# Performance work log

Hardware: AMD Instinct MI355X
Metric: run time of the kernel (lower is better)

The kernel has to match this reference:

```python
import jax, jax.numpy as jnp
import numpy as np

VOCAB, D, BLOCK = 32000, 1024, 2048
B, S = 4, 2048

def setup_inputs() -> dict:
    key = jax.random.key(0)
    ks = jax.random.split(key, 12)
    s = 0.02
    return {
        "x": jax.random.randint(ks[0], (B, S), 0, VOCAB),
        "tok_emb": jax.random.normal(ks[1], (VOCAB, D), jnp.float32) * s,
        "pos_emb": jax.random.normal(ks[2], (BLOCK, D), jnp.float32) * s,
        "Wq": jax.random.normal(ks[3], (D, D), jnp.float32) * s,
        "bq": jnp.zeros((D,), jnp.float32),
        "Wk": jax.random.normal(ks[4], (D, D), jnp.float32) * s,
        "bk": jnp.zeros((D,), jnp.float32),
        "Wv": jax.random.normal(ks[5], (D, D), jnp.float32) * s,
        "bv": jnp.zeros((D,), jnp.float32),
        "Wfc": jax.random.normal(ks[6], (VOCAB, D), jnp.float32) * s,
        "bfc": jnp.zeros((VOCAB,), jnp.float32),
    }

def reference(x, tok_emb, pos_emb, Wq, bq, Wk, bk, Wv, bv, Wfc, bfc):
    # embeddings: token lookup + learned positional
    h = tok_emb[x] + pos_emb[jnp.arange(x.shape[1])][None, :, :]  # [B,S,D]
    Q = h @ Wq.T + bq
    K = h @ Wk.T + bk
    V = h @ Wv.T + bv
    scale = 1.0 / jnp.sqrt(jnp.float32(Q.shape[-1]))
    scores = jnp.einsum('bqd,bkd->bqk', Q, K) * scale  # [B,S,S]
    attn = jax.nn.softmax(scores, axis=-1)
    out = jnp.einsum('bqk,bkd->bqd', attn, V)
    return out @ Wfc.T + bfc  # [B,S,VOCAB]
```

## Files before the change

kernel.cpp:

```cpp
#include <hip/hip_runtime.h>
#include <hip/hip_bf16.h>
#include <stdint.h>

typedef __bf16 bf16x8 __attribute__((ext_vector_type(8)));
typedef float f32x4 __attribute__((ext_vector_type(4)));
typedef unsigned short u16x8 __attribute__((ext_vector_type(8)));

#define DEVINL static __device__ __forceinline__

DEVINL unsigned short f2bf(float f) {
  unsigned u = __builtin_bit_cast(unsigned, f);
  unsigned r = (u + 0x7FFFu + ((u >> 16) & 1u)) >> 16;
  return (unsigned short)r;
}
DEVINL float bf2f(unsigned short u) {
  return __builtin_bit_cast(float, ((unsigned)u) << 16);
}

DEVINL void gload_lds16(const unsigned short* g, unsigned short* l) {
  __builtin_amdgcn_global_load_lds(
      (const __attribute__((address_space(1))) void*)g,
      (__attribute__((address_space(3))) void*)l, 16, 0, 0);
}

__global__ __launch_bounds__(256) void embed_kernel(
    const int* __restrict__ x, const float* __restrict__ tok,
    const float* __restrict__ pos, unsigned short* __restrict__ hb)
{
  const int bs = blockIdx.x;
  const int s  = bs & 2047;
  const long trow = (long)x[bs] * 1024;
  const int d = threadIdx.x * 4;
  const float4 t = *(const float4*)(tok + trow + d);
  const float4 p = *(const float4*)(pos + (long)s * 1024 + d);
  ushort4 o;
  o.x = f2bf(t.x + p.x);
  o.y = f2bf(t.y + p.y);
  o.z = f2bf(t.z + p.z);
  o.w = f2bf(t.w + p.w);
  *(ushort4*)(hb + (long)bs * 1024 + d) = o;
}

__global__ __launch_bounds__(256) void cvt4_kernel(
    const float* __restrict__ wq, const float* __restrict__ wk,
    const float* __restrict__ wv, const float* __restrict__ wfc,
    unsigned short* __restrict__ out)
{
  for (long i = blockIdx.x * blockDim.x + threadIdx.x; i < 8978432;
       i += (long)gridDim.x * blockDim.x) {
    const float* src;
    long off;
    if (i < 262144)       { src = wq;  off = i; }
    else if (i < 524288)  { src = wk;  off = i - 262144; }
    else if (i < 786432)  { src = wv;  off = i - 524288; }
    else                  { src = wfc; off = i - 786432; }
    float4 v = ((const float4*)src)[off];
    ushort4 o;
    o.x = f2bf(v.x); o.y = f2bf(v.y); o.z = f2bf(v.z); o.w = f2bf(v.w);
    ((ushort4*)out)[i] = o;
  }
}

template<int OUTMODE>
__global__ __launch_bounds__(256) void gemm_bt(
    const unsigned short* __restrict__ A, const unsigned short* __restrict__ B,
    void* __restrict__ Cout, const float* __restrict__ bias,
    float scale, int M, int N, int K,
    long sA, long sB, long sC, int Mb, long tStride, int mapMode)
{
  __shared__ __align__(16) unsigned short lA[128 * 32];
  __shared__ __align__(16) unsigned short lB[128 * 32];
  const int tid = threadIdx.x, wid = tid >> 6, lane = tid & 63;
  int bx, by, bz;
  if (mapMode == 0) {
    bx = blockIdx.x; by = blockIdx.y; bz = blockIdx.z;
  } else {
    const int bid = blockIdx.x;
    const int g = bid & 7, jj = bid >> 3;
    bz = g >> 1;
    by = (g & 1) * 8 + (jj & 7);
    bx = jj >> 3;
  }
  A += (long)bz * sA;
  B += (long)bz * sB;
  const int bm = by * 128, bn = bx * 128;

  const int c0 = wid * 64 + lane, c1 = c0 + 256;
  const unsigned short* gA0 = A + (long)(bm + (c0 >> 2)) * K + (c0 & 3) * 8;
  const unsigned short* gA1 = A + (long)(bm + (c1 >> 2)) * K + (c1 & 3) * 8;
  const unsigned short* gB0 = B + (long)(bn + (c0 >> 2)) * K + (c0 & 3) * 8;
  const unsigned short* gB1 = B + (long)(bn + (c1 >> 2)) * K + (c1 & 3) * 8;
  unsigned short* lA0 = lA + wid * 512;
  unsigned short* lA1 = lA + 2048 + wid * 512;
  unsigned short* lB0 = lB + wid * 512;
  unsigned short* lB1 = lB + 2048 + wid * 512;

  const int wr = (wid >> 1) * 64, wc = (wid & 1) * 64;
  const int lr = lane & 15, lk = (lane >> 4) * 8;

  f32x4 acc[4][4] = {};
  const int nk = K >> 5;
  for (int kt = 0; kt < nk; ++kt) {
    const int ko = kt << 5;
    gload_lds16(gA0 + ko, lA0);
    gload_lds16(gA1 + ko, lA1);
    gload_lds16(gB0 + ko, lB0);
    gload_lds16(gB1 + ko, lB1);
    __syncthreads();
    bf16x8 af[4], bg[4];
#pragma unroll
    for (int m = 0; m < 4; ++m)
      af[m] = *(const bf16x8*)(const void*)(lA + (wr + m * 16 + lr) * 32 + lk);
#pragma unroll
    for (int n = 0; n < 4; ++n)
      bg[n] = *(const bf16x8*)(const void*)(lB + (wc + n * 16 + lr) * 32 + lk);
#pragma unroll
    for (int m = 0; m < 4; ++m)
#pragma unroll
      for (int n = 0; n < 4; ++n)
        acc[m][n] = __builtin_amdgcn_mfma_f32_16x16x32_bf16(af[m], bg[n],
                                                            acc[m][n], 0, 0, 0);
    __syncthreads();
  }

  const int r0 = bm + wr + ((lane >> 4) << 2);
  const int cbase = bn + wc + lr;
#pragma unroll
  for (int n = 0; n < 4; ++n) {
    const int col = cbase + n * 16;
    const float bv = bias ? bias[col] : 0.f;
#pragma unroll
    for (int m = 0; m < 4; ++m) {
      const int row0 = r0 + m * 16;
      if (OUTMODE == 2) {
        float* C = (float*)Cout + (long)bz * sC;
#pragma unroll
        for (int i = 0; i < 4; ++i)
          C[(long)(row0 + i) * N + col] = acc[m][n][i] * scale + bv;
      } else if (OUTMODE == 0) {
        unsigned short* C = (unsigned short*)Cout + (long)bz * sC;
#pragma unroll
        for (int i = 0; i < 4; ++i)
          C[(long)(row0 + i) * N + col] = f2bf(acc[m][n][i] * scale + bv);
      } else {
        unsigned short* C = (unsigned short*)Cout;
        const int b = row0 / Mb;
        const int srow = row0 - b * Mb;
        ushort4 o;
        o.x = f2bf(acc[m][n][0] * scale + bv);
        o.y = f2bf(acc[m][n][1] * scale + bv);
        o.z = f2bf(acc[m][n][2] * scale + bv);
        o.w = f2bf(acc[m][n][3] * scale + bv);
        *(ushort4*)(C + (long)b * tStride + (long)col * Mb + srow) = o;
      }
    }
  }
}

__global__ __launch_bounds__(256) void qkv_bt(
    const unsigned short* __restrict__ A, const unsigned short* __restrict__ B,
    unsigned short* __restrict__ Qb, unsigned short* __restrict__ Kb,
    unsigned short* __restrict__ Vt,
    const float* __restrict__ bq, const float* __restrict__ bk,
    const float* __restrict__ bv)
{
  constexpr int K = 1024;
  __shared__ __align__(16) unsigned short lA[128 * 32];
  __shared__ __align__(16) unsigned short lB[128 * 32];
  const int tid = threadIdx.x, wid = tid >> 6, lane = tid & 63;
  const int bid = blockIdx.x;
  const int g = bid & 7, j = bid >> 3;
  const int bm = (g * 8 + (j & 7)) * 128;
  const int bn = (j >> 3) * 128;
  const int sector = bn >> 10;
  const int bnl = bn & 1023;

  const int c0 = wid * 64 + lane, c1 = c0 + 256;
  const unsigned short* gA0 = A + (long)(bm + (c0 >> 2)) * K + (c0 & 3) * 8;
  const unsigned short* gA1 = A + (long)(bm + (c1 >> 2)) * K + (c1 & 3) * 8;
  const unsigned short* gB0 = B + (long)(bn + (c0 >> 2)) * K + (c0 & 3) * 8;
  const unsigned short* gB1 = B + (long)(bn + (c1 >> 2)) * K + (c1 & 3) * 8;
  unsigned short* lA0 = lA + wid * 512;
  unsigned short* lA1 = lA + 2048 + wid * 512;
  unsigned short* lB0 = lB + wid * 512;
  unsigned short* lB1 = lB + 2048 + wid * 512;

  const int wr = (wid >> 1) * 64, wc = (wid & 1) * 64;
  const int lr = lane & 15, lk = (lane >> 4) * 8;

  f32x4 acc[4][4] = {};
  for (int kt = 0; kt < 32; ++kt) {
    const int ko = kt << 5;
    gload_lds16(gA0 + ko, lA0);
    gload_lds16(gA1 + ko, lA1);
    gload_lds16(gB0 + ko, lB0);
    gload_lds16(gB1 + ko, lB1);
    __syncthreads();
    bf16x8 af[4], bg[4];
#pragma unroll
    for (int m = 0; m < 4; ++m)
      af[m] = *(const bf16x8*)(const void*)(lA + (wr + m * 16 + lr) * 32 + lk);
#pragma unroll
    for (int n = 0; n < 4; ++n)
      bg[n] = *(const bf16x8*)(const void*)(lB + (wc + n * 16 + lr) * 32 + lk);
#pragma unroll
    for (int m = 0; m < 4; ++m)
#pragma unroll
      for (int n = 0; n < 4; ++n)
        acc[m][n] = __builtin_amdgcn_mfma_f32_16x16x32_bf16(af[m], bg[n],
                                                            acc[m][n], 0, 0, 0);
    __syncthreads();
  }

  const float* bias = (sector == 0) ? bq : (sector == 1) ? bk : bv;
  const int r0 = bm + wr + ((lane >> 4) << 2);
  const int cbase = bnl + wc + lr;
#pragma unroll
  for (int n = 0; n < 4; ++n) {
    const int col = cbase + n * 16;
    const float bb = bias[col];
#pragma unroll
    for (int m = 0; m < 4; ++m) {
      const int row0 = r0 + m * 16;
      if (sector == 2) {
        const int b = row0 >> 11;
        const int srow = row0 & 2047;
        ushort4 o;
        o.x = f2bf(acc[m][n][0] + bb);
        o.y = f2bf(acc[m][n][1] + bb);
        o.z = f2bf(acc[m][n][2] + bb);
        o.w = f2bf(acc[m][n][3] + bb);
        *(ushort4*)(Vt + (long)b * (1024L * 2048) + (long)col * 2048 + srow) = o;
      } else {
        unsigned short* C = (sector == 0) ? Qb : Kb;
#pragma unroll
        for (int i = 0; i < 4; ++i)
          C[(long)(row0 + i) * 1024 + col] = f2bf(acc[m][n][i] + bb);
      }
    }
  }
}

__global__ __launch_bounds__(256) void softmax_kernel(unsigned short* __restrict__ S)
{
  unsigned short* row = S + (long)blockIdx.x * 2048;
  const int t = threadIdx.x, lane = t & 63, wid = t >> 6;
  __shared__ float redm[4], reds[4];
  u16x8 raw = ((const u16x8*)row)[t];
  float v[8];
#pragma unroll
  for (int j = 0; j < 8; ++j) v[j] = bf2f(raw[j]);
  float mx = v[0];
#pragma unroll
  for (int j = 1; j < 8; ++j) mx = fmaxf(mx, v[j]);
#pragma unroll
  for (int off = 32; off; off >>= 1) mx = fmaxf(mx, __shfl_xor(mx, off, 64));
  if (lane == 0) redm[wid] = mx;
  __syncthreads();
  mx = fmaxf(fmaxf(redm[0], redm[1]), fmaxf(redm[2], redm[3]));
  float s = 0.f;
#pragma unroll
  for (int j = 0; j < 8; ++j) { v[j] = __expf(v[j] - mx); s += v[j]; }
#pragma unroll
  for (int off = 32; off; off >>= 1) s += __shfl_xor(s, off, 64);
  if (lane == 0) reds[wid] = s;
  __syncthreads();
  s = reds[0] + reds[1] + reds[2] + reds[3];
  const float inv = 1.f / s;
  u16x8 o;
#pragma unroll
  for (int j = 0; j < 8; ++j) o[j] = f2bf(v[j] * inv);
  ((u16x8*)row)[t] = o;
}

DEVINL bf16x8 ldfrag(const unsigned short* p, int row, int kx) {
  return *(const bf16x8*)((const char*)p + row * 128 + kx);
}

#define BARSB() do { __builtin_amdgcn_s_barrier(); \
                     __builtin_amdgcn_sched_barrier(0); } while (0)
#define LGK0() asm volatile("s_waitcnt lgkmcnt(0)")
#define VM6()  asm volatile("s_waitcnt vmcnt(6)")

#define MF16(rb, aArr, bArr) do { \
  _Pragma("unroll") for (int m_ = 0; m_ < 4; ++m_) \
  _Pragma("unroll") for (int n_ = 0; n_ < 4; ++n_) \
    acc[(rb) + m_][n_] = __builtin_amdgcn_mfma_f32_16x16x32_bf16( \
        aArr[m_], bArr[n_], acc[(rb) + m_][n_], 0, 0, 0); \
} while (0)

#define STG_A(b, h, gk) do { \
  const char* s_ = srcA + (h) * 262144 + (long)(((gk) & 15)) * 128; \
  gload_lds16((const unsigned short*)(s_ + la0), \
              dA + (b) * 16384 + (h) * 8192 + dO0); \
  gload_lds16((const unsigned short*)(s_ + la1), \
              dA + (b) * 16384 + (h) * 8192 + dO1); } while (0)
#define STG_B(b, h, gk) do { \
  int t_ = (gk) >> 4; if (t_ >= len) t_ = len - 1; \
  const char* s_ = Bbase + ((long)(bnStart + t_) << 19) + \
                   (h) * 262144 + (long)(((gk) & 15)) * 128; \
  gload_lds16((const unsigned short*)(s_ + la0), \
              dB + (b) * 16384 + (h) * 8192 + dO0); \
  gload_lds16((const unsigned short*)(s_ + la1), \
              dB + (b) * 16384 + (h) * 8192 + dO1); } while (0)

#define KTILE(BUF, S1, S2, S3, S4) do { \
  bf16x8 b0_[4], b1_[4], aA_[4], aB_[4], aC_[4], aD_[4]; \
  _Pragma("unroll") for (int n = 0; n < 4; ++n) { \
    b0_[n] = ldfrag(dB + (BUF) * 16384, wn * 64 + n * 16 + lr, kx0); \
    b1_[n] = ldfrag(dB + (BUF) * 16384, wn * 64 + n * 16 + lr, kx1); } \
  _Pragma("unroll") for (int m = 0; m < 4; ++m) \
    aA_[m] = ldfrag(dA + (BUF) * 16384, wm * 128 + m * 16 + lr, kx0); \
  S1; \
  BARSB(); LGK0(); __builtin_amdgcn_s_setprio(1); \
  MF16(0, aA_, b0_); \
  __builtin_amdgcn_s_setprio(0); BARSB(); \
  _Pragma("unroll") for (int m = 0; m < 4; ++m) { \
    aB_[m] = ldfrag(dA + (BUF) * 16384, wm * 128 + (4 + m) * 16 + lr, kx0); \
    aC_[m] = ldfrag(dA + (BUF) * 16384, wm * 128 + (4 + m) * 16 + lr, kx1); } \
  S2; \
  BARSB(); LGK0(); __builtin_amdgcn_s_setprio(1); \
  MF16(4, aB_, b0_); \
  __builtin_amdgcn_s_setprio(0); BARSB(); \
  _Pragma("unroll") for (int m = 0; m < 4; ++m) \
    aD_[m] = ldfrag(dA + (BUF) * 16384, wm * 128 + m * 16 + lr, kx1); \
  S3; \
  BARSB(); LGK0(); __builtin_amdgcn_s_setprio(1); \
  MF16(4, aC_, b1_); \
  __builtin_amdgcn_s_setprio(0); BARSB(); \
  S4; VM6(); \
  BARSB(); LGK0(); __builtin_amdgcn_s_setprio(1); \
  MF16(0, aD_, b1_); \
  __builtin_amdgcn_s_setprio(0); BARSB(); \
} while (0)

__global__ __launch_bounds__(512, 2) void gemm256_fc(
    const unsigned short* __restrict__ A, const unsigned short* __restrict__ B,
    float* __restrict__ C, const float* __restrict__ bias)
{
  constexpr int N = 32000;
  __shared__ __align__(16) unsigned short lds[65536];
  const int tid = threadIdx.x, wid = tid >> 6, lane = tid & 63;
  const int wm = wid >> 2, wn = wid & 3;
  const int lr = lane & 15;
  const int kq = (lane >> 4) << 4;
  const int xr = (lane & 7) << 4;
  const int kx0 = kq ^ xr;
  const int kx1 = (64 | kq) ^ xr;

  const int bid = blockIdx.x;
  const int g = bid & 7;
  const int j = bid >> 3;
  const int bm = g * 4 + (j & 3);
  const int q = j >> 2;
  const int bnStart = (q < 5) ? 16 * q : 80 + (q - 5) * 15;
  const int len = (q < 5) ? 16 : 15;

  const int loff0 = wid * 1024 + lane * 16;
  const int loff1 = loff0 + 8192;
  const int r0 = loff0 >> 7, r1 = loff1 >> 7;
  const int c0 = (loff0 & 127) ^ ((r0 & 7) << 4);
  const int c1 = (loff1 & 127) ^ ((r1 & 7) << 4);
  const long la0 = (long)r0 * 2048 + c0;
  const long la1 = (long)r1 * 2048 + c1;
  const char* srcA = (const char*)A + ((long)bm << 19);
  const char* Bbase = (const char*)B;
  unsigned short* dA = lds;
  unsigned short* dB = lds + 32768;
  const int dO0 = wid * 512, dO1 = 4096 + wid * 512;

  f32x4 acc[8][4] = {};
  float bv[4];
#pragma unroll
  for (int n = 0; n < 4; ++n)
    bv[n] = bias[(long)bnStart * 256 + wn * 64 + n * 16 + lr];

  STG_B(0, 0, 0); STG_B(0, 1, 0); STG_A(0, 0, 0); STG_A(0, 1, 0);
  STG_B(1, 0, 1); STG_B(1, 1, 1); STG_A(1, 0, 1);
  VM6();
  BARSB();

  for (int t = 0; t < len; ++t) {
#pragma unroll 1
    for (int it = 0; it < 8; ++it) {
      const int gk = t * 16 + 2 * it;
      KTILE(0, STG_A(1, 1, gk + 1), STG_B(0, 0, gk + 2), STG_B(0, 1, gk + 2),
            STG_A(0, 0, gk + 2));
      KTILE(1, STG_A(0, 1, gk + 2), STG_B(1, 0, gk + 3), STG_B(1, 1, gk + 3),
            STG_A(1, 0, gk + 3));
    }
    const long bnRow = ((long)bnStart + t) * 256;
    const int q4 = (lane >> 4) * 4;
#pragma unroll
    for (int m = 0; m < 8; ++m) {
      const long row = (long)bm * 256 + wm * 128 + m * 16 + q4;
#pragma unroll
      for (int i = 0; i < 4; ++i) {
        float* orow = C + (row + i) * (long)N;
#pragma unroll
        for (int n = 0; n < 4; ++n)
          __builtin_nontemporal_store(acc[m][n][i] + bv[n],
                                      &orow[bnRow + wn * 64 + n * 16 + lr]);
      }
    }
    VM6();
    const int tn = (t + 1 < len) ? t + 1 : t;
#pragma unroll
    for (int n = 0; n < 4; ++n)
      bv[n] = bias[((long)bnStart + tn) * 256 + wn * 64 + n * 16 + lr];
#pragma unroll
    for (int m = 0; m < 8; ++m)
#pragma unroll
      for (int n = 0; n < 4; ++n)
        acc[m][n] = f32x4{0.f, 0.f, 0.f, 0.f};
  }
}

extern "C" void kernel_launch(void* const* d_in, const int* in_sizes, int n_in,
                              void* d_out, int out_size, void* d_ws, size_t ws_size,
                              hipStream_t stream)
{
  const int*   x   = (const int*)d_in[0];
  const float* tok = (const float*)d_in[1];
  const float* pos = (const float*)d_in[2];
  const float* Wq  = (const float*)d_in[3];
  const float* bq  = (const float*)d_in[4];
  const float* Wk  = (const float*)d_in[5];
  const float* bk  = (const float*)d_in[6];
  const float* Wv  = (const float*)d_in[7];
  const float* bv  = (const float*)d_in[8];
  const float* Wfc = (const float*)d_in[9];
  const float* bfc = (const float*)d_in[10];
  float* out = (float*)d_out;

  char* ws = (char*)d_ws;
  unsigned short* hb   = (unsigned short*)(ws);
  unsigned short* Wqb  = (unsigned short*)(ws + 16777216);
  unsigned short* Wfcb = (unsigned short*)(ws + 23068672);
  unsigned short* Qb   = (unsigned short*)(ws + 88604672);
  unsigned short* Kb   = (unsigned short*)(ws + 105381888);
  unsigned short* Vt   = (unsigned short*)(ws + 122159104);
  unsigned short* Sc   = (unsigned short*)(ws + 138936320);
  unsigned short* AO   = hb;

  embed_kernel<<<8192, 256, 0, stream>>>(x, tok, pos, hb);
  cvt4_kernel<<<2048, 256, 0, stream>>>(Wq, Wk, Wv, Wfc, Wqb);

  dim3 blk(256);
  qkv_bt<<<dim3(1536), blk, 0, stream>>>(hb, Wqb, Qb, Kb, Vt, bq, bk, bv);
  gemm_bt<0><<<dim3(1024), blk, 0, stream>>>(Qb, Kb, Sc, nullptr, 0.03125f,
      2048, 2048, 1024, 2048L * 1024, 2048L * 1024, 2048L * 2048, 0, 0, 1);
  softmax_kernel<<<8192, 256, 0, stream>>>(Sc);
  gemm_bt<0><<<dim3(512), blk, 0, stream>>>(Sc, Vt, AO, nullptr, 1.f,
      2048, 1024, 2048, 2048L * 2048, 1024L * 2048, 2048L * 1024, 0, 0, 1);
  gemm256_fc<<<dim3(256), dim3(512), 0, stream>>>(AO, Wfcb, out, bfc);
}
```

Baseline: 774.0 us.

## Overlap weight conversion with embedding and score GEMM via fused launches

Splits the fp32-to-bf16 weight conversion so the QKV weights are converted by extra blocks in the embedding kernel, while the large Wfc conversion runs in extra blocks of a new scores GEMM kernel. This hides the memory-bound conversion behind other work and removes one launch. The scores GEMM becomes a specialized copy of the generic gemm_bt with constants baked in. The risk is that conversion blocks compete for bandwidth and compute units with the GEMM, and block scheduling order may serialize them anyway.

```diff
diff --git a/kernel.cpp b/kernel.cpp
--- a/kernel.cpp
+++ b/kernel.cpp
@@ -23,10 +23,27 @@
       (__attribute__((address_space(3))) void*)l, 16, 0, 0);
 }
 
-__global__ __launch_bounds__(256) void embed_kernel(
+__global__ __launch_bounds__(256) void embed_cvtq_kernel(
     const int* __restrict__ x, const float* __restrict__ tok,
-    const float* __restrict__ pos, unsigned short* __restrict__ hb)
-{
+    const float* __restrict__ pos, unsigned short* __restrict__ hb,
+    const float* __restrict__ wq, const float* __restrict__ wk,
+    const float* __restrict__ wv, unsigned short* __restrict__ wqkvb)
+{
+  if (blockIdx.x >= 8192) {
+    const int b = blockIdx.x - 8192;
+    for (long i = (long)b * 256 + threadIdx.x; i < 786432; i += 512 * 256) {
+      const float* src;
+      long off;
+      if (i < 262144)      { src = wq; off = i; }
+      else if (i < 524288) { src = wk; off = i - 262144; }
+      else                 { src = wv; off = i - 524288; }
+      float4 v = ((const float4*)src)[off];
+      ushort4 o;
+      o.x = f2bf(v.x); o.y = f2bf(v.y); o.z = f2bf(v.z); o.w = f2bf(v.w);
+      ((ushort4*)wqkvb)[i] = o;
+    }
+    return;
+  }
   const int bs = blockIdx.x;
   const int s  = bs & 2047;
   const long trow = (long)x[bs] * 1024;
@@ -39,26 +56,6 @@
   o.z = f2bf(t.z + p.z);
   o.w = f2bf(t.w + p.w);
   *(ushort4*)(hb + (long)bs * 1024 + d) = o;
-}
-
-__global__ __launch_bounds__(256) void cvt4_kernel(
-    const float* __restrict__ wq, const float* __restrict__ wk,
-    const float* __restrict__ wv, const float* __restrict__ wfc,
-    unsigned short* __restrict__ out)
-{
-  for (long i = blockIdx.x * blockDim.x + threadIdx.x; i < 8978432;
-       i += (long)gridDim.x * blockDim.x) {
-    const float* src;
-    long off;
-    if (i < 262144)       { src = wq;  off = i; }
-    else if (i < 524288)  { src = wk;  off = i - 262144; }
-    else if (i < 786432)  { src = wv;  off = i - 524288; }
-    else                  { src = wfc; off = i - 786432; }
-    float4 v = ((const float4*)src)[off];
-    ushort4 o;
-    o.x = f2bf(v.x); o.y = f2bf(v.y); o.z = f2bf(v.z); o.w = f2bf(v.w);
-    ((ushort4*)out)[i] = o;
-  }
 }
 
 template<int OUTMODE>
@@ -153,6 +150,87 @@
         o.w = f2bf(acc[m][n][3] * scale + bv);
         *(ushort4*)(C + (long)b * tStride + (long)col * Mb + srow) = o;
       }
+    }
+  }
+}
+
+__global__ __launch_bounds__(256) void scores_cvt_kernel(
+    const unsigned short* __restrict__ Qb, const unsigned short* __restrict__ Kb,
+    unsigned short* __restrict__ Sc,
+    const float* __restrict__ wfc, unsigned short* __restrict__ wfcb)
+{
+  __shared__ __align__(16) unsigned short lA[128 * 32];
+  __shared__ __align__(16) unsigned short lB[128 * 32];
+  if (blockIdx.x < 1024) {
+    for (long i = (long)blockIdx.x * 256 + threadIdx.x; i < 8192000;
+         i += 1024 * 256) {
+      float4 v = ((const float4*)wfc)[i];
+      ushort4 o;
+      o.x = f2bf(v.x); o.y = f2bf(v.y); o.z = f2bf(v.z); o.w = f2bf(v.w);
+      ((ushort4*)wfcb)[i] = o;
+    }
+    return;
+  }
+  constexpr int K = 1024, N = 2048;
+  const int tid = threadIdx.x, wid = tid >> 6, lane = tid & 63;
+  const int bid = blockIdx.x - 1024;
+  const int g = bid & 7, jj = bid >> 3;
+  const int bz = g >> 1;
+  const int by = (g & 1) * 8 + (jj & 7);
+  const int bx = jj >> 3;
+  const unsigned short* A = Qb + (long)bz * (2048L * 1024);
+  const unsigned short* B = Kb + (long)bz * (2048L * 1024);
+  unsigned short* C = Sc + (long)bz * (2048L * 2048);
+  const int bm = by * 128, bn = bx * 128;
+
+  const int c0 = wid * 64 + lane, c1 = c0 + 256;
+  const unsigned short* gA0 = A + (long)(bm + (c0 >> 2)) * K + (c0 & 3) * 8;
+  const unsigned short* gA1 = A + (long)(bm + (c1 >> 2)) * K + (c1 & 3) * 8;
+  const unsigned short* gB0 = B + (long)(bn + (c0 >> 2)) * K + (c0 & 3) * 8;
+  const unsigned short* gB1 = B + (long)(bn + (c1 >> 2)) * K + (c1 & 3) * 8;
+  unsigned short* lA0 = lA + wid * 512;
+  unsigned short* lA1 = lA + 2048 + wid * 512;
+  unsigned short* lB0 = lB + wid * 512;
+  unsigned short* lB1 = lB + 2048 + wid * 512;
+
+  const int wr = (wid >> 1) * 64, wc = (wid & 1) * 64;
+  const int lr = lane & 15, lk = (lane >> 4) * 8;
+
+  f32x4 acc[4][4] = {};
+  for (int kt = 0; kt < 32; ++kt) {
+    const int ko = kt << 5;
+    gload_lds16(gA0 + ko, lA0);
+    gload_lds16(gA1 + ko, lA1);
+    gload_lds16(gB0 + ko, lB0);
+    gload_lds16(gB1 + ko, lB1);
+    __syncthreads();
+    bf16x8 af[4], bg[4];
+#pragma unroll
+    for (int m = 0; m < 4; ++m)
+      af[m] = *(const bf16x8*)(const void*)(lA + (wr + m * 16 + lr) * 32 + lk);
+#pragma unroll
+    for (int n = 0; n < 4; ++n)
+      bg[n] = *(const bf16x8*)(const void*)(lB + (wc + n * 16 + lr) * 32 + lk);
+#pragma unroll
+    for (int m = 0; m < 4; ++m)
+#pragma unroll
+      for (int n = 0; n < 4; ++n)
+        acc[m][n] = __builtin_amdgcn_mfma_f32_16x16x32_bf16(af[m], bg[n],
+                                                            acc[m][n], 0, 0, 0);
+    __syncthreads();
+  }
+
+  const int r0 = bm + wr + ((lane >> 4) << 2);
+  const int cbase = bn + wc + lr;
+#pragma unroll
+  for (int n = 0; n < 4; ++n) {
+    const int col = cbase + n * 16;
+#pragma unroll
+    for (int m = 0; m < 4; ++m) {
+      const int row0 = r0 + m * 16;
+#pragma unroll
+      for (int i = 0; i < 4; ++i)
+        C[(long)(row0 + i) * N + col] = f2bf(acc[m][n][i] * 0.03125f);
     }
   }
 }
@@ -443,13 +521,11 @@
   unsigned short* Sc   = (unsigned short*)(ws + 138936320);
   unsigned short* AO   = hb;
 
-  embed_kernel<<<8192, 256, 0, stream>>>(x, tok, pos, hb);
-  cvt4_kernel<<<2048, 256, 0, stream>>>(Wq, Wk, Wv, Wfc, Wqb);
-
   dim3 blk(256);
+  embed_cvtq_kernel<<<dim3(8704), blk, 0, stream>>>(x, tok, pos, hb,
+                                                    Wq, Wk, Wv, Wqb);
   qkv_bt<<<dim3(1536), blk, 0, stream>>>(hb, Wqb, Qb, Kb, Vt, bq, bk, bv);
-  gemm_bt<0><<<dim3(1024), blk, 0, stream>>>(Qb, Kb, Sc, nullptr, 0.03125f,
-      2048, 2048, 1024, 2048L * 1024, 2048L * 1024, 2048L * 2048, 0, 0, 1);
+  scores_cvt_kernel<<<dim3(2048), blk, 0, stream>>>(Qb, Kb, Sc, Wfc, Wfcb);
   softmax_kernel<<<8192, 256, 0, stream>>>(Sc);
   gemm_bt<0><<<dim3(512), blk, 0, stream>>>(Sc, Vt, AO, nullptr, 1.f,
       2048, 1024, 2048, 2048L * 2048, 1024L * 2048, 2048L * 1024, 0, 0, 1);
```

Result: faster. 753.2 us (-2.7%).
